# Kernel tuning notes

Measured on AMD Instinct MI355X. Metric: run time of the kernel, lower is better.

Reference implementation:

```python
import jax, jax.numpy as jnp
import numpy as np

EMBED_DIM = 1024
NUM_HEADS = 16
D_K = EMBED_DIM // NUM_HEADS


def setup_inputs() -> dict:
    key = jax.random.key(0)
    ks = jax.random.split(key, 5)
    x = jax.random.normal(ks[0], (2, 2048, EMBED_DIM), dtype=jnp.float32)
    # kaiming_normal on 2D params: std = sqrt(2/fan_in) with fan_in = in_features
    w_qkv = jax.random.normal(ks[1], (3 * EMBED_DIM, EMBED_DIM), dtype=jnp.float32) * np.sqrt(2.0 / EMBED_DIM)
    b_qkv = jnp.zeros((3 * EMBED_DIM,), dtype=jnp.float32)
    w_o = jax.random.normal(ks[2], (EMBED_DIM, EMBED_DIM), dtype=jnp.float32) * np.sqrt(2.0 / EMBED_DIM)
    b_o = jnp.zeros((EMBED_DIM,), dtype=jnp.float32)
    return {"x": x, "w_qkv": w_qkv, "b_qkv": b_qkv, "w_o": w_o, "b_o": b_o}


def reference(x, w_qkv, b_qkv, w_o, b_o):
    B, N, C = x.shape
    qkv = x @ w_qkv.T + b_qkv  # [B,N,3C]
    q, k, v = jnp.split(qkv, 3, axis=-1)
    # [B,H,N,d_k]
    q = q.reshape(B, N, NUM_HEADS, D_K).transpose(0, 2, 1, 3)
    k = k.reshape(B, N, NUM_HEADS, D_K).transpose(0, 2, 1, 3)
    v = v.reshape(B, N, NUM_HEADS, D_K).transpose(0, 2, 1, 3)
    # NOTE: original forward scales by 1/sqrt(embed_dim), not 1/sqrt(d_k)
    scores = jnp.einsum('bhqd,bhkd->bhqk', q, k) / np.sqrt(C).astype(np.float32)
    causal = jnp.tril(jnp.ones((N, N), dtype=bool))
    scores = jnp.where(causal, scores, -jnp.inf)
    attn = jax.nn.softmax(scores, axis=-1)
    out = jnp.einsum('bhqk,bhkd->bhqd', attn, v)  # [B,H,N,d_k]
    out = out.transpose(0, 2, 1, 3).reshape(B, N, C)
    return out @ w_o.T + b_o
```

## Files before the change

kernel.cpp:

```cpp
#include <hip/hip_runtime.h>
#include <hip/hip_bf16.h>
#include <math.h>

typedef __bf16 bf16_t;
typedef __bf16 bf16x8 __attribute__((ext_vector_type(8)));
typedef __bf16 bf16x4 __attribute__((ext_vector_type(4)));
typedef __bf16 bf16x2 __attribute__((ext_vector_type(2)));
typedef float f32x4 __attribute__((ext_vector_type(4)));
typedef unsigned u32x4 __attribute__((ext_vector_type(4)));

#define SCALE_L2E 0.045084234f
#define ROUND_B 0.0028169f

#define MFMA16(a, b, c) __builtin_amdgcn_mfma_f32_16x16x32_bf16(a, b, c, 0, 0, 0)

__device__ __forceinline__ unsigned pack2(float a, float b) {
  return __builtin_amdgcn_perm(__builtin_bit_cast(unsigned, b),
                               __builtin_bit_cast(unsigned, a), 0x07060302u);
}

__global__ void convert3_f32_bf16(const float* __restrict__ a, int na,
                                  const float* __restrict__ b, int nb,
                                  const float* __restrict__ c, int nc,
                                  bf16_t* __restrict__ oa, bf16_t* __restrict__ ob,
                                  bf16_t* __restrict__ oc) {
  int i = (blockIdx.x * blockDim.x + threadIdx.x) * 8;
  const float* src;
  bf16_t* dst;
  int off;
  if (i < na) { src = a; dst = oa; off = i; }
  else if (i < na + nb) { src = b; dst = ob; off = i - na; }
  else if (i < na + nb + nc) { src = c; dst = oc; off = i - na - nb; }
  else return;
  float4 u = *(const float4*)&src[off];
  float4 v = *(const float4*)&src[off + 4];
  bf16x8 w = {(bf16_t)u.x, (bf16_t)u.y, (bf16_t)u.z, (bf16_t)u.w,
              (bf16_t)v.x, (bf16_t)v.y, (bf16_t)v.z, (bf16_t)v.w};
  *(bf16x8*)&dst[off] = w;
}

#define GLOBAL_AS __attribute__((address_space(1)))
#define LDS_AS __attribute__((address_space(3)))
__device__ __forceinline__ void g2l16(const void* g, void* l) {
  __builtin_amdgcn_global_load_lds((const GLOBAL_AS void*)g, (LDS_AS void*)l,
                                   16, 0, 0);
}

template <typename TC, int BN>
__launch_bounds__(256)
__global__ void gemm_bt_bias(const bf16_t* __restrict__ A,
                             const bf16_t* __restrict__ B,
                             const float* __restrict__ bias,
                             TC* __restrict__ C,
                             int M, int N, int K) {
  constexpr int NT = BN / 32;
  __shared__ bf16_t As[128 * 32];
  __shared__ bf16_t Bs[BN * 32];

  const int t = threadIdx.x;
  const int wave = t >> 6, lane = t & 63, quad = lane >> 4, ln = lane & 15;
  const int wm = (wave >> 1) * 64, wn = (wave & 1) * (BN / 2);
  const int m0 = blockIdx.y * 128, n0 = blockIdx.x * BN;

  const int srow = lane >> 2;
  const int schunk = ((lane & 3) ^ ((lane >> 3) & 3)) * 8;
  const bf16_t* gA0 = &A[(size_t)(m0 + wave * 32 + srow) * K + schunk];
  const bf16_t* gA1 = gA0 + (size_t)16 * K;
  bf16_t* lA0 = &As[(wave * 32) * 32];
  bf16_t* lA1 = &As[(wave * 32 + 16) * 32];
  const bf16_t* gB0 = &B[(size_t)(n0 + (BN == 128 ? wave * 32 : wave * 16) + srow) * K + schunk];
  const bf16_t* gB1 = gB0 + (size_t)16 * K;
  bf16_t* lB0 = &Bs[((BN == 128 ? wave * 32 : wave * 16)) * 32];
  bf16_t* lB1 = &Bs[(wave * 32 + 16) * 32];

  const int cslot = (quad ^ ((ln >> 1) & 3)) * 8;

  f32x4 acc[4][NT];
  for (int i = 0; i < 4; i++)
    for (int j = 0; j < NT; j++) acc[i][j] = (f32x4){0.f, 0.f, 0.f, 0.f};

  for (int k0 = 0; k0 < K; k0 += 32) {
    __syncthreads();
    g2l16(gA0 + k0, lA0);
    g2l16(gA1 + k0, lA1);
    g2l16(gB0 + k0, lB0);
    if (BN == 128) g2l16(gB1 + k0, lB1);
    __syncthreads();

    bf16x8 af[4], bfr[NT];
    for (int mt = 0; mt < 4; mt++)
      af[mt] = *(const bf16x8*)&As[(wm + mt * 16 + ln) * 32 + cslot];
    for (int nt = 0; nt < NT; nt++)
      bfr[nt] = *(const bf16x8*)&Bs[(wn + nt * 16 + ln) * 32 + cslot];
    for (int mt = 0; mt < 4; mt++)
      for (int nt = 0; nt < NT; nt++)
        acc[mt][nt] = MFMA16(af[mt], bfr[nt], acc[mt][nt]);
  }

  for (int nt = 0; nt < NT; nt++) {
    int col = n0 + wn + nt * 16 + ln;
    float bv = bias[col];
    for (int mt = 0; mt < 4; mt++) {
      int row = m0 + wm + mt * 16 + quad * 4;
      for (int r = 0; r < 4; r++)
        C[(size_t)(row + r) * N + col] = (TC)(acc[mt][nt][r] + bv);
    }
  }
}

__launch_bounds__(512, 2)
__global__ void gemm256_bt_bias(const bf16_t* __restrict__ A,
                                const bf16_t* __restrict__ B,
                                const float* __restrict__ bias,
                                bf16_t* __restrict__ C,
                                int M, int N, int K) {
  __shared__ __align__(16) bf16_t Ab[2][256 * 64];
  __shared__ __align__(16) bf16_t Bb[2][256 * 64];

  const int tid = threadIdx.x;
  const int wave = tid >> 6, lane = tid & 63, quad = lane >> 4, ln = lane & 15;
  const int wm = wave >> 2, wn = wave & 3;
  const int m0 = blockIdx.y * 256, n0 = blockIdx.x * 256;
  const int nt = K >> 6;

  const int rowoff = wave * 8 + (lane >> 3);
  const int c8 = ((lane & 7) ^ (lane >> 3)) * 8;
  const int w8row = wave * 8;
  const bf16_t* Arow0 = A + (size_t)(m0 + rowoff) * K + c8;
  const bf16_t* Brow0 = B + (size_t)(n0 + rowoff) * K + c8;

  auto stA = [&](int tl, int h) {
    const bf16_t* g = Arow0 + (size_t)(h * 128) * K + (size_t)tl * 64;
    bf16_t* l = &Ab[tl & 1][(h * 128 + w8row) * 64];
    g2l16(g, l);
    g2l16(g + (size_t)64 * K, l + 64 * 64);
  };
  auto stB = [&](int tl, int h) {
    const bf16_t* g = Brow0 + (size_t)(h * 128) * K + (size_t)tl * 64;
    bf16_t* l = &Bb[tl & 1][(h * 128 + w8row) * 64];
    g2l16(g, l);
    g2l16(g + (size_t)64 * K, l + 64 * 64);
  };

  const int cswl = (quad ^ (ln & 7)) * 8;
  const int aBase = (wm * 64 + ln) * 64;
  const int bBase = (wn * 32 + ln) * 64;

  f32x4 acc[8][4];
#pragma unroll
  for (int i = 0; i < 8; i++)
#pragma unroll
    for (int j = 0; j < 4; j++) acc[i][j] = (f32x4){0.f, 0.f, 0.f, 0.f};

  bf16x8 af[4][2], bfr[2][2];

  auto ldA4 = [&](int buf, int mh) {
#pragma unroll
    for (int mf = 0; mf < 4; ++mf)
#pragma unroll
      for (int sk = 0; sk < 2; ++sk)
        af[mf][sk] = *(const bf16x8*)&Ab[buf][mh * 8192 + aBase + mf * 1024 +
                                             (cswl ^ (sk << 5))];
  };
  auto ldB2 = [&](int buf, int nh) {
#pragma unroll
    for (int nf = 0; nf < 2; ++nf)
#pragma unroll
      for (int sk = 0; sk < 2; ++sk)
        bfr[nf][sk] = *(const bf16x8*)&Bb[buf][nh * 8192 + bBase + nf * 1024 +
                                               (cswl ^ (sk << 5))];
  };
  auto mm8 = [&](int mh, int nh) {
#pragma unroll
    for (int mf = 0; mf < 4; ++mf)
#pragma unroll
      for (int nf = 0; nf < 2; ++nf) {
        f32x4 c = acc[mh * 4 + mf][nh * 2 + nf];
        c = MFMA16(af[mf][0], bfr[nf][0], c);
        c = MFMA16(af[mf][1], bfr[nf][1], c);
        acc[mh * 4 + mf][nh * 2 + nf] = c;
      }
  };

#define PHASE_MM(MH, NH)                             \
  __builtin_amdgcn_s_barrier();                      \
  asm volatile("s_waitcnt lgkmcnt(0)" ::: "memory"); \
  __builtin_amdgcn_s_setprio(1);                     \
  mm8(MH, NH);                                       \
  __builtin_amdgcn_s_setprio(0);

  stA(0, 0); stB(0, 0); stA(0, 1); stB(0, 1);
  if (nt > 1) {
    stA(1, 0); stB(1, 0);
    asm volatile("s_waitcnt vmcnt(4)" ::: "memory");
  } else {
    asm volatile("s_waitcnt vmcnt(0)" ::: "memory");
  }
  __builtin_amdgcn_s_barrier();

  for (int tl = 0; tl < nt; ++tl) {
    const int buf = tl & 1;
    ldA4(buf, 0);
    ldB2(buf, 0);
    if (tl + 1 < nt) stA(tl + 1, 1);
    PHASE_MM(0, 0)
    __builtin_amdgcn_s_barrier();
    ldB2(buf, 1);
    if (tl + 1 < nt) stB(tl + 1, 1);
    PHASE_MM(0, 1)
    __builtin_amdgcn_s_barrier();
    ldA4(buf, 1);
    ldB2(buf, 0);
    if (tl + 2 < nt) stA(tl + 2, 0);
    PHASE_MM(1, 0)
    __builtin_amdgcn_s_barrier();
    ldB2(buf, 1);
    if (tl + 2 < nt) stB(tl + 2, 0);
    PHASE_MM(1, 1)
    asm volatile("s_waitcnt vmcnt(4)" ::: "memory");
    __builtin_amdgcn_s_barrier();
  }
#undef PHASE_MM

#pragma unroll
  for (int nf4 = 0; nf4 < 4; ++nf4) {
    const int col = n0 + (nf4 >> 1) * 128 + wn * 32 + (nf4 & 1) * 16 + ln;
    const float bv = bias[col];
#pragma unroll
    for (int mf8 = 0; mf8 < 8; ++mf8) {
      const int row = m0 + (mf8 >> 2) * 128 + wm * 64 + (mf8 & 3) * 16 + quad * 4;
#pragma unroll
      for (int r = 0; r < 4; ++r)
        C[(size_t)(row + r) * N + col] = (bf16_t)(acc[mf8][nf4][r] + bv);
    }
  }
}

__launch_bounds__(256, 2)
__global__ void attn_kernel(const bf16_t* __restrict__ qkv,
                            bf16_t* __restrict__ out) {
  constexpr int KP = 72, VP = 72;
  constexpr int BUF = 64 * KP;
  __shared__ __align__(16) bf16_t KsB[2 * BUF];
  __shared__ __align__(16) bf16_t VtB[2 * BUF];

  const int t = threadIdx.x;
  const int wave = t >> 6, lane = t & 63, quad = lane >> 4, ln = lane & 15;
  const int p = blockIdx.x >> 5;
  const int bh = blockIdx.x & 31;
  const int b = bh >> 4, h = bh & 15;
  const int qA = p * 64, qB = (31 - p) * 64;
  const int ntiles = 32 - p;
  const size_t rs = 3072;
  const size_t base = (size_t)b * 2048 * rs;

  const size_t qoffA = base + (size_t)(qA + wave * 16 + ln) * rs + h * 64;
  const size_t qoffB = base + (size_t)(qB + wave * 16 + ln) * rs + h * 64;
  bf16x8 qfA0 = *(const bf16x8*)&qkv[qoffA + quad * 8];
  bf16x8 qfA1 = *(const bf16x8*)&qkv[qoffA + 32 + quad * 8];
  bf16x8 qfB0 = *(const bf16x8*)&qkv[qoffB + quad * 8];
  bf16x8 qfB1 = *(const bf16x8*)&qkv[qoffB + 32 + quad * 8];

  f32x4 oA[4], oB[4];
  float lAx = 0.f, lBx = 0.f;
  for (int ct = 0; ct < 4; ct++) {
    oA[ct] = (f32x4){0.f, 0.f, 0.f, 0.f};
    oB[ct] = (f32x4){0.f, 0.f, 0.f, 0.f};
  }

  const int r0 = t >> 3, c0 = (t & 7) * 8;
  const int ksA = r0 * KP + (((t & 7) + wave) & 7) * 8;
  const int ksB2 = (r0 + 32) * KP + (((t & 7) + wave + 4) & 7) * 8;
  const int vkoff = ((((r0 >> 2) + (t & 7)) & 7)) * 8 + 2 * (r0 & 3);

  const bf16_t* kpa = &qkv[base + 1024 + h * 64 + (size_t)r0 * rs + c0];
  const bf16_t* kpb = kpa + (size_t)32 * rs;
  const bf16_t* vpa = &qkv[base + 2048 + h * 64 + (size_t)(2 * r0) * rs + c0];
  const bf16_t* vpb = vpa + rs;
  const size_t tstep = (size_t)64 * rs;

  bf16x8 ka = *(const bf16x8*)kpa; kpa += tstep;
  bf16x8 kb = *(const bf16x8*)kpb; kpb += tstep;
  bf16x8 va2 = *(const bf16x8*)vpa; vpa += tstep;
  bf16x8 vb2 = *(const bf16x8*)vpb; vpb += tstep;

  const int qgA = qA + wave * 16 + ln;
  const int qgB = qB + wave * 16 + ln;

  auto stage_to = [&](int buf) {
    bf16_t* KsW = &KsB[buf * BUF];
    bf16_t* VtW = &VtB[buf * BUF];
    *(bf16x8*)&KsW[ksA] = ka;
    *(bf16x8*)&KsW[ksB2] = kb;
#pragma unroll
    for (int j = 0; j < 8; j++) {
      bf16x2 w2 = {va2[j], vb2[j]};
      *(bf16x2*)&VtW[(c0 + j) * VP + vkoff] = w2;
    }
  };
  auto prefetch = [&]() {
    ka = *(const bf16x8*)kpa; kpa += tstep;
    kb = *(const bf16x8*)kpb; kpb += tstep;
    va2 = *(const bf16x8*)vpa; vpa += tstep;
    vb2 = *(const bf16x8*)vpb; vpb += tstep;
  };
  auto load_kfs = [&](const bf16_t* Ks, bf16x8* kf0s, bf16x8* kf1s) {
#pragma unroll
    for (int st = 0; st < 4; st++) {
      const int krow = st * 16 + ln;
      const int rot = 2 * st + (ln >> 3);
      kf0s[st] = *(const bf16x8*)&Ks[krow * KP + ((quad + rot) & 7) * 8];
      kf1s[st] = *(const bf16x8*)&Ks[krow * KP + ((quad + 4 + rot) & 7) * 8];
    }
  };
  auto qk_block = [&](const bf16x8* kf0s, const bf16x8* kf1s, bf16x8 q0,
                      bf16x8 q1, float& lx, bf16x8* Bp, bool masked,
                      int kbase, int qg) {
#pragma unroll
    for (int pr = 0; pr < 2; pr++) {
      u32x4 u;
#pragma unroll
      for (int sh = 0; sh < 2; sh++) {
        const int st = pr * 2 + sh;
        f32x4 s = (f32x4){0.f, 0.f, 0.f, 0.f};
        __builtin_amdgcn_s_setprio(1);
        s = MFMA16(kf0s[st], q0, s);
        s = MFMA16(kf1s[st], q1, s);
        __builtin_amdgcn_s_setprio(0);
        const int k0g = kbase + st * 16 + quad * 4;
        float pv[4];
#pragma unroll
        for (int r = 0; r < 4; r++) {
          float e = __builtin_amdgcn_exp2f(fmaf(s[r], SCALE_L2E, ROUND_B));
          if (masked && (k0g + r > qg)) e = 0.f;
          lx += e;
          pv[r] = e;
        }
        u[sh * 2] = pack2(pv[0], pv[1]);
        u[sh * 2 + 1] = pack2(pv[2], pv[3]);
      }
      Bp[pr] = __builtin_bit_cast(bf16x8, u);
    }
  };
  auto load_vfs = [&](const bf16_t* Vt, bf16x8* A8s) {
#pragma unroll
    for (int pr = 0; pr < 2; pr++) {
#pragma unroll
      for (int ct = 0; ct < 4; ct++) {
        const int dd = ct * 16 + ln;
        const int bc = (quad >> 1) + 2 * ct + (ln >> 3);
        const int cA = (4 * pr + bc) & 7;
        const int cB = (4 * pr + 2 + bc) & 7;
        bf16x4 v0 = *(const bf16x4*)&Vt[dd * VP + cA * 8 + (quad & 1) * 4];
        bf16x4 v1 = *(const bf16x4*)&Vt[dd * VP + cB * 8 + (quad & 1) * 4];
        A8s[pr * 4 + ct] = __builtin_shufflevector(v0, v1, 0, 1, 2, 3, 4, 5, 6, 7);
      }
    }
  };

  auto body = [&](int kt, bool hasA, bool maskA, bool maskB) {
    if (kt + 1 < ntiles) {
      stage_to((kt + 1) & 1);
      if (kt + 2 < ntiles) prefetch();
    }
    const bf16_t* Ks = &KsB[(kt & 1) * BUF];
    const bf16_t* Vt = &VtB[(kt & 1) * BUF];
    bf16x8 kf0s[4], kf1s[4];
    load_kfs(Ks, kf0s, kf1s);
    bf16x8 BpA[2], BpB[2];
    if (hasA) qk_block(kf0s, kf1s, qfA0, qfA1, lAx, BpA, maskA, kt * 64, qgA);
    qk_block(kf0s, kf1s, qfB0, qfB1, lBx, BpB, maskB, kt * 64, qgB);
    bf16x8 A8s[8];
    load_vfs(Vt, A8s);
    __builtin_amdgcn_s_setprio(1);
#pragma unroll
    for (int pr = 0; pr < 2; pr++) {
#pragma unroll
      for (int ct = 0; ct < 4; ct++) {
        if (hasA) oA[ct] = MFMA16(A8s[pr * 4 + ct], BpA[pr], oA[ct]);
        oB[ct] = MFMA16(A8s[pr * 4 + ct], BpB[pr], oB[ct]);
      }
    }
    __builtin_amdgcn_s_setprio(0);
    if (kt + 1 < ntiles) __syncthreads();
  };

  stage_to(0);
  if (ntiles > 1) prefetch();
  __syncthreads();

  for (int kt = 0; kt < p; kt++) body(kt, true, false, false);
  body(p, true, true, false);
  for (int kt = p + 1; kt < 31 - p; kt++) body(kt, false, false, false);
  body(31 - p, false, false, true);

  lAx += __shfl_xor(lAx, 16);
  lAx += __shfl_xor(lAx, 32);
  lBx += __shfl_xor(lBx, 16);
  lBx += __shfl_xor(lBx, 32);
  const float invA = __builtin_amdgcn_rcpf(lAx);
  const float invB = __builtin_amdgcn_rcpf(lBx);
  const int ocol = h * 64 + quad * 4;
#pragma unroll
  for (int ct = 0; ct < 4; ct++) {
    bf16x4 wa, wb;
#pragma unroll
    for (int r = 0; r < 4; r++) {
      wa[r] = (bf16_t)(oA[ct][r] * invA);
      wb[r] = (bf16_t)(oB[ct][r] * invB);
    }
    *(bf16x4*)&out[(size_t)(b * 2048 + qgA) * 1024 + ocol + ct * 16] = wa;
    *(bf16x4*)&out[(size_t)(b * 2048 + qgB) * 1024 + ocol + ct * 16] = wb;
  }
}

extern "C" void kernel_launch(void* const* d_in, const int* in_sizes, int n_in,
                              void* d_out, int out_size, void* d_ws, size_t ws_size,
                              hipStream_t stream) {
  const float* x     = (const float*)d_in[0];
  const float* w_qkv = (const float*)d_in[1];
  const float* b_qkv = (const float*)d_in[2];
  const float* w_o   = (const float*)d_in[3];
  const float* b_o   = (const float*)d_in[4];
  float* out = (float*)d_out;

  bf16_t* qkv   = (bf16_t*)d_ws;
  bf16_t* xbf   = qkv + (size_t)4096 * 3072;
  bf16_t* wqkvb = xbf + (size_t)4096 * 1024;
  bf16_t* wob   = wqkvb + (size_t)3072 * 1024;
  bf16_t* attn  = xbf;

  const int na = 4096 * 1024, nb = 3072 * 1024, nc = 1024 * 1024;
  convert3_f32_bf16<<<dim3((na + nb + nc) / (256 * 8)), 256, 0, stream>>>(
      x, na, w_qkv, nb, w_o, nc, xbf, wqkvb, wob);

  gemm256_bt_bias<<<dim3(3072 / 256, 4096 / 256), 512, 0, stream>>>(
      xbf, wqkvb, b_qkv, qkv, 4096, 3072, 1024);
  attn_kernel<<<dim3(512), 256, 0, stream>>>(qkv, attn);
  gemm_bt_bias<float, 64><<<dim3(1024 / 64, 4096 / 128), 256, 0, stream>>>(
      attn, wob, b_o, out, 4096, 1024, 1024);
}
```

Measured before the change: 175.5 us.

## Split paired causal query tiles into one tile per block, longest first

Replaces the paired-query-tile scheme, where each block handled tiles p and 31-p to balance causal work, with one 64-row query tile per block. The grid doubles to 1024 blocks, ordered heaviest first so that the longest tiles start early. Launch bounds are raised to 4 blocks per SIMD to allow more occupancy. In exchange, K/V tiles are no longer shared across two query tiles, so K/V staging traffic per unit of work goes up, and the raised launch bound may limit registers.

After: 176.4 us. No clear change (+0.5%).

```diff
diff --git a/kernel.cpp b/kernel.cpp
--- a/kernel.cpp
+++ b/kernel.cpp
@@ -236,7 +236,7 @@
   }
 }
 
-__launch_bounds__(256, 2)
+__launch_bounds__(256, 4)
 __global__ void attn_kernel(const bf16_t* __restrict__ qkv,
                             bf16_t* __restrict__ out) {
   constexpr int KP = 72, VP = 72;
@@ -246,27 +246,21 @@
 
   const int t = threadIdx.x;
   const int wave = t >> 6, lane = t & 63, quad = lane >> 4, ln = lane & 15;
-  const int p = blockIdx.x >> 5;
+  const int qt = 31 - (blockIdx.x >> 5);
   const int bh = blockIdx.x & 31;
   const int b = bh >> 4, h = bh & 15;
-  const int qA = p * 64, qB = (31 - p) * 64;
-  const int ntiles = 32 - p;
+  const int q0 = qt * 64;
+  const int ntiles = qt + 1;
   const size_t rs = 3072;
   const size_t base = (size_t)b * 2048 * rs;
 
-  const size_t qoffA = base + (size_t)(qA + wave * 16 + ln) * rs + h * 64;
-  const size_t qoffB = base + (size_t)(qB + wave * 16 + ln) * rs + h * 64;
-  bf16x8 qfA0 = *(const bf16x8*)&qkv[qoffA + quad * 8];
-  bf16x8 qfA1 = *(const bf16x8*)&qkv[qoffA + 32 + quad * 8];
-  bf16x8 qfB0 = *(const bf16x8*)&qkv[qoffB + quad * 8];
-  bf16x8 qfB1 = *(const bf16x8*)&qkv[qoffB + 32 + quad * 8];
-
-  f32x4 oA[4], oB[4];
-  float lAx = 0.f, lBx = 0.f;
-  for (int ct = 0; ct < 4; ct++) {
-    oA[ct] = (f32x4){0.f, 0.f, 0.f, 0.f};
-    oB[ct] = (f32x4){0.f, 0.f, 0.f, 0.f};
-  }
+  const size_t qoff = base + (size_t)(q0 + wave * 16 + ln) * rs + h * 64;
+  bf16x8 qf0 = *(const bf16x8*)&qkv[qoff + quad * 8];
+  bf16x8 qf1 = *(const bf16x8*)&qkv[qoff + 32 + quad * 8];
+
+  f32x4 o[4];
+  float lx = 0.f;
+  for (int ct = 0; ct < 4; ct++) o[ct] = (f32x4){0.f, 0.f, 0.f, 0.f};
 
   const int r0 = t >> 3, c0 = (t & 7) * 8;
   const int ksA = r0 * KP + (((t & 7) + wave) & 7) * 8;
@@ -284,8 +278,7 @@
   bf16x8 va2 = *(const bf16x8*)vpa; vpa += tstep;
   bf16x8 vb2 = *(const bf16x8*)vpb; vpb += tstep;
 
-  const int qgA = qA + wave * 16 + ln;
-  const int qgB = qB + wave * 16 + ln;
+  const int qg = q0 + wave * 16 + ln;
 
   auto stage_to = [&](int buf) {
     bf16_t* KsW = &KsB[buf * BUF];
@@ -313,9 +306,8 @@
       kf1s[st] = *(const bf16x8*)&Ks[krow * KP + ((quad + 4 + rot) & 7) * 8];
     }
   };
-  auto qk_block = [&](const bf16x8* kf0s, const bf16x8* kf1s, bf16x8 q0,
-                      bf16x8 q1, float& lx, bf16x8* Bp, bool masked,
-                      int kbase, int qg) {
+  auto qk_block = [&](const bf16x8* kf0s, const bf16x8* kf1s, bf16x8* Bp,
+                      bool masked, int kbase) {
 #pragma unroll
     for (int pr = 0; pr < 2; pr++) {
       u32x4 u;
@@ -324,8 +316,8 @@
         const int st = pr * 2 + sh;
         f32x4 s = (f32x4){0.f, 0.f, 0.f, 0.f};
         __builtin_amdgcn_s_setprio(1);
-        s = MFMA16(kf0s[st], q0, s);
-        s = MFMA16(kf1s[st], q1, s);
+        s = MFMA16(kf0s[st], qf0, s);
+        s = MFMA16(kf1s[st], qf1, s);
         __builtin_amdgcn_s_setprio(0);
         const int k0g = kbase + st * 16 + quad * 4;
         float pv[4];
@@ -358,7 +350,7 @@
     }
   };
 
-  auto body = [&](int kt, bool hasA, bool maskA, bool maskB) {
+  auto body = [&](int kt, bool masked) {
     if (kt + 1 < ntiles) {
       stage_to((kt + 1) & 1);
       if (kt + 2 < ntiles) prefetch();
@@ -367,19 +359,16 @@
     const bf16_t* Vt = &VtB[(kt & 1) * BUF];
     bf16x8 kf0s[4], kf1s[4];
     load_kfs(Ks, kf0s, kf1s);
-    bf16x8 BpA[2], BpB[2];
-    if (hasA) qk_block(kf0s, kf1s, qfA0, qfA1, lAx, BpA, maskA, kt * 64, qgA);
-    qk_block(kf0s, kf1s, qfB0, qfB1, lBx, BpB, maskB, kt * 64, qgB);
+    bf16x8 Bp[2];
+    qk_block(kf0s, kf1s, Bp, masked, kt * 64);
     bf16x8 A8s[8];
     load_vfs(Vt, A8s);
     __builtin_amdgcn_s_setprio(1);
 #pragma unroll
     for (int pr = 0; pr < 2; pr++) {
 #pragma unroll
-      for (int ct = 0; ct < 4; ct++) {
-        if (hasA) oA[ct] = MFMA16(A8s[pr * 4 + ct], BpA[pr], oA[ct]);
-        oB[ct] = MFMA16(A8s[pr * 4 + ct], BpB[pr], oB[ct]);
-      }
+      for (int ct = 0; ct < 4; ct++)
+        o[ct] = MFMA16(A8s[pr * 4 + ct], Bp[pr], o[ct]);
     }
     __builtin_amdgcn_s_setprio(0);
     if (kt + 1 < ntiles) __syncthreads();
@@ -389,28 +378,19 @@
   if (ntiles > 1) prefetch();
   __syncthreads();
 
-  for (int kt = 0; kt < p; kt++) body(kt, true, false, false);
-  body(p, true, true, false);
-  for (int kt = p + 1; kt < 31 - p; kt++) body(kt, false, false, false);
-  body(31 - p, false, false, true);
-
-  lAx += __shfl_xor(lAx, 16);
-  lAx += __shfl_xor(lAx, 32);
-  lBx += __shfl_xor(lBx, 16);
-  lBx += __shfl_xor(lBx, 32);
-  const float invA = __builtin_amdgcn_rcpf(lAx);
-  const float invB = __builtin_amdgcn_rcpf(lBx);
+  for (int kt = 0; kt < qt; kt++) body(kt, false);
+  body(qt, true);
+
+  lx += __shfl_xor(lx, 16);
+  lx += __shfl_xor(lx, 32);
+  const float inv = __builtin_amdgcn_rcpf(lx);
   const int ocol = h * 64 + quad * 4;
 #pragma unroll
   for (int ct = 0; ct < 4; ct++) {
-    bf16x4 wa, wb;
-#pragma unroll
-    for (int r = 0; r < 4; r++) {
-      wa[r] = (bf16_t)(oA[ct][r] * invA);
-      wb[r] = (bf16_t)(oB[ct][r] * invB);
-    }
-    *(bf16x4*)&out[(size_t)(b * 2048 + qgA) * 1024 + ocol + ct * 16] = wa;
-    *(bf16x4*)&out[(size_t)(b * 2048 + qgB) * 1024 + ocol + ct * 16] = wb;
+    bf16x4 w;
+#pragma unroll
+    for (int r = 0; r < 4; r++) w[r] = (bf16_t)(o[ct][r] * inv);
+    *(bf16x4*)&out[(size_t)(b * 2048 + qg) * 1024 + ocol + ct * 16] = w;
   }
 }
 
@@ -436,7 +416,7 @@
 
   gemm256_bt_bias<<<dim3(3072 / 256, 4096 / 256), 512, 0, stream>>>(
       xbf, wqkvb, b_qkv, qkv, 4096, 3072, 1024);
-  attn_kernel<<<dim3(512), 256, 0, stream>>>(qkv, attn);
+  attn_kernel<<<dim3(1024), 256, 0, stream>>>(qkv, attn);
   gemm_bt_bias<float, 64><<<dim3(1024 / 64, 4096 / 128), 256, 0, stream>>>(
       attn, wob, b_o, out, 4096, 1024, 1024);
 }
```
